# Performance work log

Hardware: AMD Instinct MI355X
Metric: run time of the kernel (lower is better)

Reference implementation:

```python
import jax, jax.numpy as jnp
import numpy as np

N_NODES = 100000
N_GRAPHS = 64


def gcn_layer(x, src, dst, W, b, n):
    # GCNConv: h = x @ W; out_i = sum_j norm_ij * h_j (+ self loop), + bias
    h = x @ W
    deg = jax.ops.segment_sum(jnp.ones(src.shape[0], x.dtype), dst, num_segments=n)
    dinv = jnp.where(deg > 0, jax.lax.rsqrt(deg), 0.0)
    norm = dinv[src] * dinv[dst]                      # [E+N]
    agg = jax.ops.segment_sum(h[src] * norm[:, None], dst, num_segments=n)
    return agg + b


def setup_inputs() -> dict:
    key = jax.random.key(0)
    ks = jax.random.split(key, 12)
    nfeat, nhid, nclass = 128, 64, 10
    E = 1600000
    x = jax.random.normal(ks[0], (N_NODES, nfeat), dtype=jnp.float32)
    edge_index = jax.random.randint(ks[1], (2, E), 0, N_NODES, dtype=jnp.int64)
    batch = jnp.sort(jax.random.randint(ks[2], (N_NODES,), 0, N_GRAPHS, dtype=jnp.int64))
    def w(k, fi, fo):
        return jax.random.normal(k, (fi, fo), dtype=jnp.float32) / np.sqrt(fi)
    return {
        "x": x, "edge_index": edge_index, "batch": batch,
        "W1": w(ks[3], nfeat, nhid), "b1": jnp.zeros((nhid,), jnp.float32),
        "W2": w(ks[4], nhid, nhid), "b2": jnp.zeros((nhid,), jnp.float32),
        "W3": w(ks[5], nhid, nhid), "b3": jnp.zeros((nhid,), jnp.float32),
        "Wl": w(ks[6], nhid, nclass), "bl": jnp.zeros((nclass,), jnp.float32),
    }


def reference(x, edge_index, batch, W1, b1, W2, b2, W3, b3, Wl, bl):
    n = x.shape[0]
    loop = jnp.arange(n, dtype=edge_index.dtype)
    src = jnp.concatenate([edge_index[0], loop])   # self-loops appended
    dst = jnp.concatenate([edge_index[1], loop])
    h = x  # eval mode: dropout is identity; use_bn=False
    for W, b in ((W1, b1), (W2, b2), (W3, b3)):
        h = jax.nn.relu(gcn_layer(h, src, dst, W, b, n))
    # global mean pool per graph
    sums = jax.ops.segment_sum(h, batch, num_segments=N_GRAPHS)
    cnts = jax.ops.segment_sum(jnp.ones((n,), h.dtype), batch, num_segments=N_GRAPHS)
    pooled = sums / jnp.maximum(cnts, 1.0)[:, None]   # [G, nhid]
    logits = pooled @ Wl + bl
    return jax.nn.softmax(logits, axis=1)
```

## Files before the change

kernel.cpp:

```cpp
#include <hip/hip_runtime.h>
#include <math.h>


typedef __attribute__((ext_vector_type(8))) short bf16x8;
typedef __attribute__((ext_vector_type(4))) float f32x4;
typedef __attribute__((ext_vector_type(2))) float f32x2;

__device__ __forceinline__ unsigned short f2bf(float f) {
    unsigned int u = __float_as_uint(f);
    u += 0x7fffu + ((u >> 16) & 1u);
    return (unsigned short)(u >> 16);
}
__device__ __forceinline__ float bf2f(unsigned short u) {
    return __uint_as_float((unsigned int)u << 16);
}
__device__ __forceinline__ float bflo(unsigned int u) {
    return __uint_as_float(u << 16);
}
__device__ __forceinline__ float bfhi(unsigned int u) {
    return __uint_as_float(u & 0xffff0000u);
}


__global__ __launch_bounds__(256) void hist_kernel(const int* __restrict__ dst,
                                                   int* __restrict__ counts,
                                                   int E, int P, int C,
                                                   const float* __restrict__ W1,
                                                   const float* __restrict__ W2,
                                                   const float* __restrict__ W3,
                                                   unsigned short* __restrict__ Wt1,
                                                   unsigned short* __restrict__ Wt2,
                                                   unsigned short* __restrict__ Wt3,
                                                   float* __restrict__ sums, int G) {
    int t = threadIdx.x, b = blockIdx.x;
    if (b >= 256) {
        int xb = b - 256;
        if (xb < 3) {
            const float* W = (xb == 0) ? W1 : ((xb == 1) ? W2 : W3);
            unsigned short* Wt = (xb == 0) ? Wt1 : ((xb == 1) ? Wt2 : Wt3);
            int K = (xb == 0) ? 128 : 64;
            int o = t & 63;
            for (int k = t >> 6; k < K; k += 4)
                Wt[o * K + k] = f2bf(W[k * 64 + o]);
        } else {
            for (int i = t; i < G * 65; i += 256) sums[i] = 0.f;
        }
        return;
    }
    __shared__ int hist[256];
    if (t < P) hist[t] = 0;
    __syncthreads();
    int beg = b * C, end = min(E, beg + C);
    for (int e = beg + t; e < end; e += 256)
        atomicAdd(&hist[dst[e] >> 9], 1);
    __syncthreads();
    if (t < P) counts[t * 256 + b] = hist[t];
}

__global__ __launch_bounds__(256) void pscan_kernel(const int* __restrict__ counts,
                                                    int* __restrict__ pbase,
                                                    int P) {
    __shared__ int s[256];
    int t = threadIdx.x;
    int v = 0;
    if (t < P)
        for (int b = 0; b < 256; ++b) v += counts[t * 256 + b];
    s[t] = v;
    __syncthreads();
    for (int off = 1; off < 256; off <<= 1) {
        int u = (t >= off) ? s[t - off] : 0;
        __syncthreads();
        s[t] += u;
        __syncthreads();
    }
    if (t < P) pbase[t] = s[t] - v;
    if (t == 255) pbase[P] = s[255];
}

__global__ __launch_bounds__(256) void offs_kernel(const int* __restrict__ counts,
                                                   const int* __restrict__ pbase,
                                                   int* __restrict__ offs) {
    __shared__ int s[256];
    int t = threadIdx.x, p = blockIdx.x;
    int v = counts[p * 256 + t];
    s[t] = v;
    __syncthreads();
    for (int off = 1; off < 256; off <<= 1) {
        int u = (t >= off) ? s[t - off] : 0;
        __syncthreads();
        s[t] += u;
        __syncthreads();
    }
    offs[p * 256 + t] = pbase[p] + s[t] - v;
}

__global__ __launch_bounds__(256) void bin_kernel(const int* __restrict__ src,
                                                  const int* __restrict__ dst,
                                                  const int* __restrict__ offs,
                                                  unsigned int* __restrict__ binned,
                                                  int E, int P, int C) {
    __shared__ int cur[256];
    int t = threadIdx.x, b = blockIdx.x;
    if (t < P) cur[t] = offs[t * 256 + b];
    __syncthreads();
    int beg = b * C, end = min(E, beg + C);
    for (int e = beg + t; e < end; e += 256) {
        int d = dst[e], s = src[e];
        int pos = atomicAdd(&cur[d >> 9], 1);
        binned[pos] = ((unsigned int)s << 9) | (unsigned int)(d & 511);
    }
}

__global__ __launch_bounds__(512) void lsortA_kernel(const unsigned int* __restrict__ binned,
                                                     const int* __restrict__ pbase,
                                                     int* __restrict__ rowptr,
                                                     float* __restrict__ dinv,
                                                     int* __restrict__ partTot8, int N) {
    __shared__ int ldeg[512];
    __shared__ int s[512];
    int t = threadIdx.x, p = blockIdx.x;
    int lo = p << 9;
    ldeg[t] = 0;
    __syncthreads();
    int eBeg = pbase[p], eEnd = pbase[p + 1];
    for (int j = eBeg + t; j < eEnd; j += 512)
        atomicAdd(&ldeg[binned[j] & 511u], 1);
    __syncthreads();
    int real = ldeg[t];
    int a = (lo + t < N) ? ((real + 1 + 7) & ~7) : 0;
    s[t] = a;
    __syncthreads();
    for (int off = 1; off < 512; off <<= 1) {
        int u = (t >= off) ? s[t - off] : 0;
        __syncthreads();
        s[t] += u;
        __syncthreads();
    }
    if (lo + t < N) {
        rowptr[lo + t] = s[t] - a;
        dinv[lo + t] = rsqrtf((float)(real + 1));
    }
    if (t == 511) partTot8[p] = s[511];
}

__global__ __launch_bounds__(256) void lsortB_kernel(const unsigned int* __restrict__ binned,
                                                     const int* __restrict__ pbase,
                                                     const int* __restrict__ partTot8,
                                                     int* __restrict__ rowptr,
                                                     const float* __restrict__ dinv,
                                                     float2* __restrict__ csrw, int N, int P) {
    __shared__ int s[256];
    __shared__ int srow[513];
    __shared__ int cur[512];
    __shared__ float sdi[512];
    int t = threadIdx.x, p = blockIdx.x;
    int v = (t < P) ? partTot8[t] : 0;
    s[t] = v;
    __syncthreads();
    for (int off = 1; off < 256; off <<= 1) {
        int u = (t >= off) ? s[t - off] : 0;
        __syncthreads();
        s[t] += u;
        __syncthreads();
    }
    int b8 = s[p] - partTot8[p];
    int endP = s[p];
    if (p == 0 && t == 0) rowptr[N] = s[P - 1];
    int lo = p << 9, span = min(N - lo, 512);
    for (int i = t; i < span; i += 256) {
        int r = rowptr[lo + i] + b8;
        srow[i] = r;
        cur[i] = r;
        sdi[i] = dinv[lo + i];
        rowptr[lo + i] = r;
    }
    if (t == 0) srow[span] = endP;
    __syncthreads();
    int eBeg = pbase[p], eEnd = pbase[p + 1];
    for (int j = eBeg + t; j < eEnd; j += 256) {
        unsigned int vv = binned[j];
        int sr = (int)(vv >> 9);
        int dl = (int)(vv & 511u);
        int pos = atomicAdd(&cur[dl], 1);
        csrw[pos] = make_float2(__int_as_float(sr << 7), dinv[sr] * sdi[dl]);
    }
    __syncthreads();
    for (int i = t; i < span; i += 256) {
        int c = cur[i];
        float d = sdi[i];
        csrw[c] = make_float2(__int_as_float((lo + i) << 7), d * d);
        int nxt = srow[i + 1];
        for (int k = c + 1; k < nxt; ++k)
            csrw[k] = make_float2(0.f, 0.f);
    }
}

template <int FIN, bool F32IN>
__global__ __launch_bounds__(256) void gemm_mfma_kernel(const void* __restrict__ Xv,
                                                        const unsigned short* __restrict__ Wt,
                                                        unsigned short* __restrict__ H,
                                                        int N) {
    constexpr int KS = FIN / 32;
    constexpr int LDP = FIN + 8;
    __shared__ unsigned short sX[64 * LDP];
    int tid = threadIdx.x;
    int rowBase = blockIdx.x * 64;

    if (F32IN) {
        for (int i = tid * 4; i < 64 * FIN; i += 1024) {
            int r = i / FIN, c = i - r * FIN;
            int gr = min(rowBase + r, N - 1);
            float4 vv = *(const float4*)((const float*)Xv + (size_t)gr * FIN + c);
            unsigned e0 = __float_as_uint(vv.x) + 0x8000u, e1 = __float_as_uint(vv.y) + 0x8000u;
            unsigned e2 = __float_as_uint(vv.z) + 0x8000u, e3 = __float_as_uint(vv.w) + 0x8000u;
            uint2 pk;
            pk.x = __builtin_amdgcn_perm(e1, e0, 0x07060302);
            pk.y = __builtin_amdgcn_perm(e3, e2, 0x07060302);
            *(uint2*)&sX[r * LDP + c] = pk;
        }
    } else {
        for (int i = tid * 8; i < 64 * FIN; i += 2048) {
            int r = i / FIN, c = i - r * FIN;
            int gr = min(rowBase + r, N - 1);
            uint4 vv = *(const uint4*)((const unsigned short*)Xv + (size_t)gr * FIN + c);
            *(uint4*)&sX[r * LDP + c] = vv;
        }
    }
    __syncthreads();

    int wave = tid >> 6;
    int lane = tid & 63;
    int r = lane & 15, g = lane >> 4;
    int node = rowBase + wave * 16 + r;

    bf16x8 afr[4][KS];
#pragma unroll
    for (int m = 0; m < 4; ++m)
#pragma unroll
        for (int s = 0; s < KS; ++s)
            afr[m][s] = *(const bf16x8*)&Wt[(m * 16 + r) * FIN + s * 32 + g * 8];

    f32x4 acc[4];
#pragma unroll
    for (int m = 0; m < 4; ++m) acc[m] = (f32x4){0.f, 0.f, 0.f, 0.f};

#pragma unroll
    for (int s = 0; s < KS; ++s) {
        bf16x8 bfr = *(const bf16x8*)&sX[(wave * 16 + r) * LDP + s * 32 + g * 8];
#pragma unroll
        for (int m = 0; m < 4; ++m)
            acc[m] = __builtin_amdgcn_mfma_f32_16x16x32_bf16(afr[m][s], bfr, acc[m], 0, 0, 0);
    }

    if (node < N) {
#pragma unroll
        for (int m = 0; m < 4; ++m) {
            ushort4 o;
            o.x = f2bf(acc[m][0]); o.y = f2bf(acc[m][1]);
            o.z = f2bf(acc[m][2]); o.w = f2bf(acc[m][3]);
            *(ushort4*)&H[(size_t)node * 64 + m * 16 + g * 4] = o;
        }
    }
}

template <int NQ>
__device__ __forceinline__ void gstep(const float2* __restrict__ csrw,
                                      const char* __restrict__ hb,
                                      int e, int g, int fo, f32x2 acc[4]) {
    float2 c[NQ];
#pragma unroll
    for (int q = 0; q < NQ; ++q) c[q] = csrw[e + 8 * q + g];
    uint4 u[NQ];
#pragma unroll
    for (int q = 0; q < NQ; ++q)
        u[q] = *(const uint4*)(hb + __float_as_int(c[q].x) + fo);
#pragma unroll
    for (int q = 0; q < NQ; ++q) {
        f32x2 w2;
        w2.x = c[q].y; w2.y = c[q].y;
        acc[0] = __builtin_elementwise_fma(w2, (f32x2){bflo(u[q].x), bfhi(u[q].x)}, acc[0]);
        acc[1] = __builtin_elementwise_fma(w2, (f32x2){bflo(u[q].y), bfhi(u[q].y)}, acc[1]);
        acc[2] = __builtin_elementwise_fma(w2, (f32x2){bflo(u[q].z), bfhi(u[q].z)}, acc[2]);
        acc[3] = __builtin_elementwise_fma(w2, (f32x2){bflo(u[q].w), bfhi(u[q].w)}, acc[3]);
    }
}

__global__ __launch_bounds__(256) void gather_kernel(const float2* __restrict__ csrw,
                                                     const int* __restrict__ rowptr,
                                                     const unsigned short* __restrict__ h,
                                                     const float* __restrict__ b,
                                                     unsigned short* __restrict__ aggb, int N) {
    int node = (blockIdx.x * 256 + threadIdx.x) >> 6;
    int lane = threadIdx.x & 63;
    if (node >= N) return;
    int g = lane >> 3;
    int f = lane & 7;
    int fo = f * 16;
    int beg = rowptr[node], end = rowptr[node + 1];

    f32x2 acc[4];
#pragma unroll
    for (int k = 0; k < 4; ++k) acc[k] = (f32x2){0.f, 0.f};

    const char* hb = (const char*)h;
    int e = beg;
    int nb = (end - beg) >> 3;
    while (nb > 4) { gstep<4>(csrw, hb, e, g, fo, acc); e += 32; nb -= 4; }
    if (nb == 4)      gstep<4>(csrw, hb, e, g, fo, acc);
    else if (nb == 3) gstep<3>(csrw, hb, e, g, fo, acc);
    else if (nb == 2) gstep<2>(csrw, hb, e, g, fo, acc);
    else              gstep<1>(csrw, hb, e, g, fo, acc);

    float a[8];
#pragma unroll
    for (int k = 0; k < 4; ++k) { a[2 * k] = acc[k].x; a[2 * k + 1] = acc[k].y; }
#pragma unroll
    for (int k = 0; k < 8; ++k) {
        float v = a[k];
        v += __shfl_xor(v, 8);
        v += __shfl_xor(v, 16);
        v += __shfl_xor(v, 32);
        a[k] = v;
    }
    if (g == 0) {
        float4 bv0 = *(const float4*)&b[f * 8];
        float4 bv1 = *(const float4*)&b[f * 8 + 4];
        float a0 = fmaxf(a[0] + bv0.x, 0.f), a1 = fmaxf(a[1] + bv0.y, 0.f);
        float a2 = fmaxf(a[2] + bv0.z, 0.f), a3 = fmaxf(a[3] + bv0.w, 0.f);
        float a4 = fmaxf(a[4] + bv1.x, 0.f), a5 = fmaxf(a[5] + bv1.y, 0.f);
        float a6 = fmaxf(a[6] + bv1.z, 0.f), a7 = fmaxf(a[7] + bv1.w, 0.f);
        uint4 o;
        o.x = ((unsigned)f2bf(a1) << 16) | f2bf(a0);
        o.y = ((unsigned)f2bf(a3) << 16) | f2bf(a2);
        o.z = ((unsigned)f2bf(a5) << 16) | f2bf(a4);
        o.w = ((unsigned)f2bf(a7) << 16) | f2bf(a6);
        *(uint4*)&aggb[((size_t)node << 6) + f * 8] = o;
    }
}

__global__ __launch_bounds__(256) void pool_kernel(const unsigned short* __restrict__ hb,
                                                   const int* __restrict__ batch,
                                                   float* __restrict__ sums,
                                                   float* __restrict__ cnts, int N) {
    int lane = threadIdx.x & 63;
    int wid = (blockIdx.x * 256 + threadIdx.x) >> 6;
    int base = wid * 32;
    if (base >= N) return;
    int nn = min(N - base, 32);
    int bl = batch[base + min(lane & 31, nn - 1)];

    float v[32];
#pragma unroll
    for (int j = 0; j < 32; ++j) {
        int node = base + min(j, nn - 1);
        v[j] = bf2f(hb[(size_t)node * 64 + lane]);
    }

    int curg = __shfl(bl, 0);
    float acc = 0.f, cnt = 0.f;
#pragma unroll
    for (int j = 0; j < 32; ++j) {
        if (j < nn) {
            int g = __shfl(bl, j);
            if (g != curg) {
                atomicAdd(&sums[curg * 64 + lane], acc);
                if (lane == 0) atomicAdd(&cnts[curg], cnt);
                acc = 0.f; cnt = 0.f; curg = g;
            }
            acc += v[j]; cnt += 1.f;
        }
    }
    atomicAdd(&sums[curg * 64 + lane], acc);
    if (lane == 0) atomicAdd(&cnts[curg], cnt);
}

__global__ void final_kernel(const float* __restrict__ sums, const float* __restrict__ cnts,
                             const float* __restrict__ Wl, const float* __restrict__ bl,
                             float* __restrict__ out, int G) {
    int g = blockIdx.x * blockDim.x + threadIdx.x;
    if (g >= G) return;
    float inv = 1.0f / fmaxf(cnts[g], 1.0f);
    float logits[10];
#pragma unroll
    for (int k = 0; k < 10; ++k) logits[k] = bl[k];
    for (int c = 0; c < 64; ++c) {
        float p = sums[g * 64 + c] * inv;
#pragma unroll
        for (int k = 0; k < 10; ++k) logits[k] = fmaf(p, Wl[c * 10 + k], logits[k]);
    }
    float m = logits[0];
#pragma unroll
    for (int k = 1; k < 10; ++k) m = fmaxf(m, logits[k]);
    float se = 0.f;
#pragma unroll
    for (int k = 0; k < 10; ++k) { logits[k] = expf(logits[k] - m); se += logits[k]; }
    float is = 1.0f / se;
#pragma unroll
    for (int k = 0; k < 10; ++k) out[g * 10 + k] = logits[k] * is;
}

extern "C" void kernel_launch(void* const* d_in, const int* in_sizes, int n_in,
                              void* d_out, int out_size, void* d_ws, size_t ws_size,
                              hipStream_t stream) {
    const float* x    = (const float*)d_in[0];
    const int* edges  = (const int*)d_in[1];
    const int* batch  = (const int*)d_in[2];
    const float* W1   = (const float*)d_in[3];
    const float* b1   = (const float*)d_in[4];
    const float* W2   = (const float*)d_in[5];
    const float* b2   = (const float*)d_in[6];
    const float* W3   = (const float*)d_in[7];
    const float* b3   = (const float*)d_in[8];
    const float* Wl   = (const float*)d_in[9];
    const float* bl   = (const float*)d_in[10];

    const int N = in_sizes[0] / 128;
    const int E = in_sizes[1] / 2;
    const int G = out_size / 10;
    const int* src = edges;
    const int* dst = edges + E;

    float* ws     = (float*)d_ws;
    unsigned short* h = (unsigned short*)ws;
    unsigned short* aggb = (unsigned short*)(ws + (size_t)N * 64);
    unsigned int* binned = (unsigned int*)ws;
    size_t csrwOff = (size_t)2 * N * 64;
    float2* csrw  = (float2*)(ws + csrwOff);
    size_t o = csrwOff + (size_t)2 * (E + 8 * N);
    float* dinv   = ws + o;            o += N;
    int*   rowptr = (int*)(ws + o);    o += N + 1;
    int*   counts = (int*)(ws + o);    o += 256 * 256;
    int*   offs   = (int*)(ws + o);    o += 256 * 256;
    int*   pbase  = (int*)(ws + o);    o += 257;
    float* sums   = ws + o;            o += (size_t)G * 64;
    float* cnts   = ws + o;            o += G;
    int*   partTot8 = (int*)(ws + o);  o += 256;
    unsigned short* Wt1 = (unsigned short*)(ws + o);
    unsigned short* Wt2 = Wt1 + 64 * 128;
    unsigned short* Wt3 = Wt2 + 64 * 64;

    const int gemmGrid = (N + 63) / 64;
    const int gatherGrid = (N + 3) / 4;
    const int poolGrid = ((N + 31) / 32 + 3) / 4;
    const int P = (N + 511) >> 9;
    const int C = (E + 255) / 256;

    hist_kernel<<<260, 256, 0, stream>>>(dst, counts, E, P, C,
                                         W1, W2, W3, Wt1, Wt2, Wt3, sums, G);
    pscan_kernel<<<1, 256, 0, stream>>>(counts, pbase, P);
    offs_kernel<<<P, 256, 0, stream>>>(counts, pbase, offs);
    bin_kernel<<<256, 256, 0, stream>>>(src, dst, offs, binned, E, P, C);
    lsortA_kernel<<<P, 512, 0, stream>>>(binned, pbase, rowptr, dinv, partTot8, N);
    lsortB_kernel<<<P, 256, 0, stream>>>(binned, pbase, partTot8, rowptr, dinv, csrw, N, P);

    gemm_mfma_kernel<128, true><<<gemmGrid, 256, 0, stream>>>(x, Wt1, h, N);
    gather_kernel<<<gatherGrid, 256, 0, stream>>>(csrw, rowptr, h, b1, aggb, N);

    gemm_mfma_kernel<64, false><<<gemmGrid, 256, 0, stream>>>(aggb, Wt2, h, N);
    gather_kernel<<<gatherGrid, 256, 0, stream>>>(csrw, rowptr, h, b2, aggb, N);

    gemm_mfma_kernel<64, false><<<gemmGrid, 256, 0, stream>>>(aggb, Wt3, h, N);
    gather_kernel<<<gatherGrid, 256, 0, stream>>>(csrw, rowptr, h, b3, aggb, N);

    pool_kernel<<<poolGrid, 256, 0, stream>>>(aggb, batch, sums, cnts, N);
    final_kernel<<<1, 64, 0, stream>>>(sums, cnts, Wl, bl, (float*)d_out, G);
}
```

Before: 358.7 us.

## Replace CSR rowptr layout with fixed 24-slot ELL rows plus overflow

Switches the neighbor list from a prefix-scanned CSR with padded rows to a hybrid layout: each node gets 24 fixed slots, and higher-degree nodes spill into a per-partition overflow area addressed by a packed word. This removes the cross-partition scan in lsortB and the rowptr loads and variable-length loop dispatch in the gather, which always runs a fixed 3-step gather plus an optional overflow loop. In exchange it pads low-degree nodes to 24 entries. With an average degree around 17 that means more zero-weight gathers and more index memory traffic. It also moves aggb to a new workspace offset.

```diff
diff --git a/kernel.cpp b/kernel.cpp
--- a/kernel.cpp
+++ b/kernel.cpp
@@ -113,9 +113,8 @@
 
 __global__ __launch_bounds__(512) void lsortA_kernel(const unsigned int* __restrict__ binned,
                                                      const int* __restrict__ pbase,
-                                                     int* __restrict__ rowptr,
                                                      float* __restrict__ dinv,
-                                                     int* __restrict__ partTot8, int N) {
+                                                     int* __restrict__ ovfw, int N) {
     __shared__ int ldeg[512];
     __shared__ int s[512];
     int t = threadIdx.x, p = blockIdx.x;
@@ -127,8 +126,10 @@
         atomicAdd(&ldeg[binned[j] & 511u], 1);
     __syncthreads();
     int real = ldeg[t];
-    int a = (lo + t < N) ? ((real + 1 + 7) & ~7) : 0;
-    s[t] = a;
+    int deg1 = real + 1;
+    int ovfUsed = (lo + t < N) ? max(deg1 - 24, 0) : 0;
+    int gsl = ((ovfUsed + 7) >> 3) << 3;
+    s[t] = gsl;
     __syncthreads();
     for (int off = 1; off < 512; off <<= 1) {
         int u = (t >= off) ? s[t - off] : 0;
@@ -137,61 +138,55 @@
         __syncthreads();
     }
     if (lo + t < N) {
-        rowptr[lo + t] = s[t] - a;
-        dinv[lo + t] = rsqrtf((float)(real + 1));
-    }
-    if (t == 511) partTot8[p] = s[511];
+        dinv[lo + t] = rsqrtf((float)deg1);
+        int obase = ((eBeg + 7) & ~7) + (p << 12);
+        int base = obase + (s[t] - gsl);
+        ovfw[lo + t] = gsl ? (((base >> 3) << 7) | (gsl >> 3)) : 0;
+    }
 }
 
 __global__ __launch_bounds__(256) void lsortB_kernel(const unsigned int* __restrict__ binned,
                                                      const int* __restrict__ pbase,
-                                                     const int* __restrict__ partTot8,
-                                                     int* __restrict__ rowptr,
+                                                     const int* __restrict__ ovfw,
                                                      const float* __restrict__ dinv,
-                                                     float2* __restrict__ csrw, int N, int P) {
-    __shared__ int s[256];
-    __shared__ int srow[513];
+                                                     float2* __restrict__ csrw,
+                                                     float2* __restrict__ ovf, int N) {
     __shared__ int cur[512];
     __shared__ float sdi[512];
+    __shared__ int sov[512];
     int t = threadIdx.x, p = blockIdx.x;
-    int v = (t < P) ? partTot8[t] : 0;
-    s[t] = v;
-    __syncthreads();
-    for (int off = 1; off < 256; off <<= 1) {
-        int u = (t >= off) ? s[t - off] : 0;
-        __syncthreads();
-        s[t] += u;
-        __syncthreads();
-    }
-    int b8 = s[p] - partTot8[p];
-    int endP = s[p];
-    if (p == 0 && t == 0) rowptr[N] = s[P - 1];
     int lo = p << 9, span = min(N - lo, 512);
     for (int i = t; i < span; i += 256) {
-        int r = rowptr[lo + i] + b8;
-        srow[i] = r;
-        cur[i] = r;
+        cur[i] = 0;
         sdi[i] = dinv[lo + i];
-        rowptr[lo + i] = r;
-    }
-    if (t == 0) srow[span] = endP;
+        sov[i] = ovfw[lo + i];
+    }
     __syncthreads();
     int eBeg = pbase[p], eEnd = pbase[p + 1];
     for (int j = eBeg + t; j < eEnd; j += 256) {
         unsigned int vv = binned[j];
         int sr = (int)(vv >> 9);
         int dl = (int)(vv & 511u);
-        int pos = atomicAdd(&cur[dl], 1);
-        csrw[pos] = make_float2(__int_as_float(sr << 7), dinv[sr] * sdi[dl]);
+        int i = atomicAdd(&cur[dl], 1);
+        float2 ent = make_float2(__int_as_float(sr << 7), dinv[sr] * sdi[dl]);
+        if (i < 24) csrw[(size_t)(lo + dl) * 24 + i] = ent;
+        else        ovf[(size_t)((sov[dl] >> 7) << 3) + i - 24] = ent;
     }
     __syncthreads();
     for (int i = t; i < span; i += 256) {
-        int c = cur[i];
+        int real = cur[i];
+        int node = lo + i;
         float d = sdi[i];
-        csrw[c] = make_float2(__int_as_float((lo + i) << 7), d * d);
-        int nxt = srow[i + 1];
-        for (int k = c + 1; k < nxt; ++k)
-            csrw[k] = make_float2(0.f, 0.f);
+        float2 self = make_float2(__int_as_float(node << 7), d * d);
+        int deg1 = real + 1;
+        int ob = (sov[i] >> 7) << 3;
+        if (real < 24) csrw[(size_t)node * 24 + real] = self;
+        else           ovf[(size_t)ob + real - 24] = self;
+        for (int k = deg1; k < 24; ++k)
+            csrw[(size_t)node * 24 + k] = make_float2(0.f, 0.f);
+        int gsl = (sov[i] & 127) << 3;
+        for (int k = max(deg1 - 24, 0); k < gsl; ++k)
+            ovf[(size_t)ob + k] = make_float2(0.f, 0.f);
     }
 }
 
@@ -286,7 +281,8 @@
 }
 
 __global__ __launch_bounds__(256) void gather_kernel(const float2* __restrict__ csrw,
-                                                     const int* __restrict__ rowptr,
+                                                     const float2* __restrict__ ovf,
+                                                     const int* __restrict__ ovfw,
                                                      const unsigned short* __restrict__ h,
                                                      const float* __restrict__ b,
                                                      unsigned short* __restrict__ aggb, int N) {
@@ -296,20 +292,23 @@
     int g = lane >> 3;
     int f = lane & 7;
     int fo = f * 16;
-    int beg = rowptr[node], end = rowptr[node + 1];
 
     f32x2 acc[4];
 #pragma unroll
     for (int k = 0; k < 4; ++k) acc[k] = (f32x2){0.f, 0.f};
 
     const char* hb = (const char*)h;
-    int e = beg;
-    int nb = (end - beg) >> 3;
-    while (nb > 4) { gstep<4>(csrw, hb, e, g, fo, acc); e += 32; nb -= 4; }
-    if (nb == 4)      gstep<4>(csrw, hb, e, g, fo, acc);
-    else if (nb == 3) gstep<3>(csrw, hb, e, g, fo, acc);
-    else if (nb == 2) gstep<2>(csrw, hb, e, g, fo, acc);
-    else              gstep<1>(csrw, hb, e, g, fo, acc);
+    gstep<3>(csrw, hb, node * 24, g, fo, acc);
+
+    int ow = ovfw[node];
+    if (ow) {
+        int onb = ow & 127;
+        int oe = (ow >> 7) << 3;
+        while (onb >= 4) { gstep<4>(ovf, hb, oe, g, fo, acc); oe += 32; onb -= 4; }
+        if (onb == 3)      gstep<3>(ovf, hb, oe, g, fo, acc);
+        else if (onb == 2) gstep<2>(ovf, hb, oe, g, fo, acc);
+        else if (onb == 1) gstep<1>(ovf, hb, oe, g, fo, acc);
+    }
 
     float a[8];
 #pragma unroll
@@ -422,19 +421,18 @@
 
     float* ws     = (float*)d_ws;
     unsigned short* h = (unsigned short*)ws;
-    unsigned short* aggb = (unsigned short*)(ws + (size_t)N * 64);
+    unsigned short* aggb = (unsigned short*)(ws + (size_t)N * 32);
     unsigned int* binned = (unsigned int*)ws;
-    size_t csrwOff = (size_t)2 * N * 64;
-    float2* csrw  = (float2*)(ws + csrwOff);
-    size_t o = csrwOff + (size_t)2 * (E + 8 * N);
+    size_t o = (size_t)N * 64;
+    float2* csrw  = (float2*)(ws + o);  o += (size_t)48 * N;
+    float2* ovf   = (float2*)(ws + o);  o += (size_t)2 * (E + 4096 * 256 + 8);
     float* dinv   = ws + o;            o += N;
-    int*   rowptr = (int*)(ws + o);    o += N + 1;
+    int*   ovfw   = (int*)(ws + o);    o += N;
     int*   counts = (int*)(ws + o);    o += 256 * 256;
     int*   offs   = (int*)(ws + o);    o += 256 * 256;
     int*   pbase  = (int*)(ws + o);    o += 257;
     float* sums   = ws + o;            o += (size_t)G * 64;
     float* cnts   = ws + o;            o += G;
-    int*   partTot8 = (int*)(ws + o);  o += 256;
     unsigned short* Wt1 = (unsigned short*)(ws + o);
     unsigned short* Wt2 = Wt1 + 64 * 128;
     unsigned short* Wt3 = Wt2 + 64 * 64;
@@ -450,17 +448,17 @@
     pscan_kernel<<<1, 256, 0, stream>>>(counts, pbase, P);
     offs_kernel<<<P, 256, 0, stream>>>(counts, pbase, offs);
     bin_kernel<<<256, 256, 0, stream>>>(src, dst, offs, binned, E, P, C);
-    lsortA_kernel<<<P, 512, 0, stream>>>(binned, pbase, rowptr, dinv, partTot8, N);
-    lsortB_kernel<<<P, 256, 0, stream>>>(binned, pbase, partTot8, rowptr, dinv, csrw, N, P);
+    lsortA_kernel<<<P, 512, 0, stream>>>(binned, pbase, dinv, ovfw, N);
+    lsortB_kernel<<<P, 256, 0, stream>>>(binned, pbase, ovfw, dinv, csrw, ovf, N);
 
     gemm_mfma_kernel<128, true><<<gemmGrid, 256, 0, stream>>>(x, Wt1, h, N);
-    gather_kernel<<<gatherGrid, 256, 0, stream>>>(csrw, rowptr, h, b1, aggb, N);
+    gather_kernel<<<gatherGrid, 256, 0, stream>>>(csrw, ovf, ovfw, h, b1, aggb, N);
 
     gemm_mfma_kernel<64, false><<<gemmGrid, 256, 0, stream>>>(aggb, Wt2, h, N);
-    gather_kernel<<<gatherGrid, 256, 0, stream>>>(csrw, rowptr, h, b2, aggb, N);
+    gather_kernel<<<gatherGrid, 256, 0, stream>>>(csrw, ovf, ovfw, h, b2, aggb, N);
 
     gemm_mfma_kernel<64, false><<<gemmGrid, 256, 0, stream>>>(aggb, Wt3, h, N);
-    gather_kernel<<<gatherGrid, 256, 0, stream>>>(csrw, rowptr, h, b3, aggb, N);
+    gather_kernel<<<gatherGrid, 256, 0, stream>>>(csrw, ovf, ovfw, h, b3, aggb, N);
 
     pool_kernel<<<poolGrid, 256, 0, stream>>>(aggb, batch, sums, cnts, N);
     final_kernel<<<1, 64, 0, stream>>>(sums, cnts, Wl, bl, (float*)d_out, G);
```

Measured after the change: 346.9 us. 1.03x faster.
